# Performance work log

Measured on AMD Instinct MI355X. Metric: run time of the kernel, lower is better.

The kernel has to match this reference:

```python
import jax, jax.numpy as jnp
import numpy as np


def setup_inputs() -> dict:
    key = jax.random.key(0)
    k1, k2 = jax.random.split(key)
    N1, N2 = 16384, 16384
    pos1 = jax.random.normal(k1, (N1, 2), dtype=jnp.float32)
    pos2 = jax.random.normal(k2, (N2, 2), dtype=jnp.float32)
    return {"pos1": pos1, "pos2": pos2}


def reference(pos1, pos2):
    # pos1: [N1, 2], pos2: [N2, 2]
    diff = pos1[:, None, :] - pos2[None, :, :]          # [N1, N2, 2]
    dist = jnp.sqrt(jnp.sum(diff * diff, axis=2))       # [N1, N2]
    nearest = jnp.min(dist, axis=1)                     # [N1]
    return jnp.mean(nearest)
```

## Files before the change

### kernel.cpp

```cpp
#include <hip/hip_runtime.h>
#include <math.h>

#define N1 16384
#define N2 16384
#define BLOCK 256
#define PTS 8
#define I_BLOCKS (N1 / (BLOCK * PTS))
#define MAX_SLICE_N 1024

__global__ __launch_bounds__(BLOCK)
void nn_partial(const float2* __restrict__ pos1,
                const float2* __restrict__ pos2,
                float* __restrict__ partials,
                int slice_n) {
    __shared__ float4 sp[MAX_SLICE_N];
    const int ib = blockIdx.x;
    const int sl = blockIdx.y;
    const int t  = threadIdx.x;

    for (int j = t; j < slice_n; j += BLOCK) {
        float2 q = pos2[sl * slice_n + j];
        sp[j] = make_float4(-2.f * q.x, -2.f * q.y,
                            fmaf(q.x, q.x, q.y * q.y), 0.f);
    }
    __syncthreads();

    const int i0 = ib * (BLOCK * PTS) + t;
    float x[PTS], y[PTS], m[PTS];
#pragma unroll
    for (int k = 0; k < PTS; ++k) {
        float2 p = pos1[i0 + k * BLOCK];
        x[k] = p.x;
        y[k] = p.y;
        m[k] = 3.4e38f;
    }

#pragma unroll 2
    for (int j = 0; j < slice_n; ++j) {
        float4 q = sp[j];
#pragma unroll
        for (int k = 0; k < PTS; ++k) {
            float g = fmaf(x[k], q.x, fmaf(y[k], q.y, q.z));
            m[k] = fminf(m[k], g);
        }
    }

#pragma unroll
    for (int k = 0; k < PTS; ++k) {
        partials[(size_t)sl * N1 + i0 + k * BLOCK] = m[k];
    }
}

__global__ __launch_bounds__(BLOCK)
void nn_reduce(const float* __restrict__ partials,
               const float2* __restrict__ pos1,
               float* __restrict__ blocksums,
               int slices) {
    const int t = threadIdx.x;
    const int i = blockIdx.x * BLOCK + t;

    float m = 3.4e38f;
    for (int s = 0; s < slices; ++s) {
        m = fminf(m, partials[(size_t)s * N1 + i]);
    }
    float2 p = pos1[i];
    float d2 = fmaxf(fmaf(p.x, p.x, p.y * p.y) + m, 0.f);
    float sum = sqrtf(d2);

    for (int off = 32; off > 0; off >>= 1) {
        sum += __shfl_down(sum, off, 64);
    }
    __shared__ float wsum[BLOCK / 64];
    if ((t & 63) == 0) wsum[t >> 6] = sum;
    __syncthreads();
    if (t == 0) {
        float s = 0.f;
        for (int w = 0; w < BLOCK / 64; ++w) s += wsum[w];
        blocksums[blockIdx.x] = s;
    }
}

__global__ __launch_bounds__(64)
void nn_final(const float* __restrict__ blocksums,
              float* __restrict__ out, int nblk) {
    const int t = threadIdx.x;
    float sum = (t < nblk) ? blocksums[t] : 0.f;
    for (int off = 32; off > 0; off >>= 1) {
        sum += __shfl_down(sum, off, 64);
    }
    if (t == 0) out[0] = sum / (float)N1;
}

extern "C" void kernel_launch(void* const* d_in, const int* in_sizes, int n_in,
                              void* d_out, int out_size, void* d_ws, size_t ws_size,
                              hipStream_t stream) {
    const float2* pos1 = (const float2*)d_in[0];
    const float2* pos2 = (const float2*)d_in[1];
    float* out = (float*)d_out;
    float* partials = (float*)d_ws;

    const int nblk2 = N1 / BLOCK;
    int slices = 64;
    while (slices > 1 &&
           (size_t)slices * N1 * sizeof(float) + nblk2 * sizeof(float) > ws_size)
        slices >>= 1;
    while (N2 / slices > MAX_SLICE_N) slices <<= 1;
    const int slice_n = N2 / slices;

    float* blocksums = partials + (size_t)slices * N1;

    dim3 grid1(I_BLOCKS, slices);
    nn_partial<<<grid1, BLOCK, 0, stream>>>(pos1, pos2, partials, slice_n);
    nn_reduce<<<nblk2, BLOCK, 0, stream>>>(partials, pos1, blocksums, slices);
    nn_final<<<1, 64, 0, stream>>>(blocksums, out, nblk2);
}
```

Baseline: 87.41 us.

## Unroll inner loop by 8, double slice count, fold final reduce via ticket

The inner distance loop is unrolled by 8, with a batch of shared-memory points loaded up front to expose more ILP. The number of pos2 slices goes from 64 to 128, doubling grid parallelism for the partial kernel at the cost of more partial writes and reads in the reduce. The separate final kernel launch is removed: the last reduce block, detected with an atomic ticket that the first partial block resets, sums the block results. This saves one launch but adds an atomic and a threadfence.

Result: slower. 95.41 us (+9.2%).

```diff
diff --git a/kernel.cpp b/kernel.cpp
--- a/kernel.cpp
+++ b/kernel.cpp
@@ -7,16 +7,20 @@
 #define PTS 8
 #define I_BLOCKS (N1 / (BLOCK * PTS))
 #define MAX_SLICE_N 1024
+#define UJ 8
 
 __global__ __launch_bounds__(BLOCK)
 void nn_partial(const float2* __restrict__ pos1,
                 const float2* __restrict__ pos2,
                 float* __restrict__ partials,
+                unsigned int* __restrict__ ticket,
                 int slice_n) {
     __shared__ float4 sp[MAX_SLICE_N];
     const int ib = blockIdx.x;
     const int sl = blockIdx.y;
     const int t  = threadIdx.x;
+
+    if (ib == 0 && sl == 0 && t == 0) *ticket = 0;
 
     for (int j = t; j < slice_n; j += BLOCK) {
         float2 q = pos2[sl * slice_n + j];
@@ -35,13 +39,17 @@
         m[k] = 3.4e38f;
     }
 
-#pragma unroll 2
-    for (int j = 0; j < slice_n; ++j) {
-        float4 q = sp[j];
+    for (int j = 0; j < slice_n; j += UJ) {
+        float4 qb[UJ];
 #pragma unroll
-        for (int k = 0; k < PTS; ++k) {
-            float g = fmaf(x[k], q.x, fmaf(y[k], q.y, q.z));
-            m[k] = fminf(m[k], g);
+        for (int u = 0; u < UJ; ++u) qb[u] = sp[j + u];
+#pragma unroll
+        for (int u = 0; u < UJ; ++u) {
+#pragma unroll
+            for (int k = 0; k < PTS; ++k) {
+                float g = fmaf(x[k], qb[u].x, fmaf(y[k], qb[u].y, qb[u].z));
+                m[k] = fminf(m[k], g);
+            }
         }
     }
 
@@ -55,6 +63,8 @@
 void nn_reduce(const float* __restrict__ partials,
                const float2* __restrict__ pos1,
                float* __restrict__ blocksums,
+               unsigned int* __restrict__ ticket,
+               float* __restrict__ out,
                int slices) {
     const int t = threadIdx.x;
     const int i = blockIdx.x * BLOCK + t;
@@ -71,24 +81,26 @@
         sum += __shfl_down(sum, off, 64);
     }
     __shared__ float wsum[BLOCK / 64];
+    __shared__ int lastflag;
     if ((t & 63) == 0) wsum[t >> 6] = sum;
     __syncthreads();
     if (t == 0) {
         float s = 0.f;
         for (int w = 0; w < BLOCK / 64; ++w) s += wsum[w];
         blocksums[blockIdx.x] = s;
+        __threadfence();
+        unsigned int old = atomicAdd(ticket, 1u);
+        lastflag = (old == gridDim.x - 1) ? 1 : 0;
     }
-}
-
-__global__ __launch_bounds__(64)
-void nn_final(const float* __restrict__ blocksums,
-              float* __restrict__ out, int nblk) {
-    const int t = threadIdx.x;
-    float sum = (t < nblk) ? blocksums[t] : 0.f;
-    for (int off = 32; off > 0; off >>= 1) {
-        sum += __shfl_down(sum, off, 64);
+    __syncthreads();
+    if (lastflag && t < 64) {
+        volatile float* vb = (volatile float*)blocksums;
+        float v = vb[t];
+        for (int off = 32; off > 0; off >>= 1) {
+            v += __shfl_down(v, off, 64);
+        }
+        if (t == 0) out[0] = v / (float)N1;
     }
-    if (t == 0) out[0] = sum / (float)N1;
 }
 
 extern "C" void kernel_launch(void* const* d_in, const int* in_sizes, int n_in,
@@ -100,17 +112,17 @@
     float* partials = (float*)d_ws;
 
     const int nblk2 = N1 / BLOCK;
-    int slices = 64;
+    int slices = 128;
     while (slices > 1 &&
-           (size_t)slices * N1 * sizeof(float) + nblk2 * sizeof(float) > ws_size)
+           (size_t)slices * N1 * sizeof(float) + (nblk2 + 1) * sizeof(float) > ws_size)
         slices >>= 1;
     while (N2 / slices > MAX_SLICE_N) slices <<= 1;
     const int slice_n = N2 / slices;
 
     float* blocksums = partials + (size_t)slices * N1;
+    unsigned int* ticket = (unsigned int*)(blocksums + nblk2);
 
     dim3 grid1(I_BLOCKS, slices);
-    nn_partial<<<grid1, BLOCK, 0, stream>>>(pos1, pos2, partials, slice_n);
-    nn_reduce<<<nblk2, BLOCK, 0, stream>>>(partials, pos1, blocksums, slices);
-    nn_final<<<1, 64, 0, stream>>>(blocksums, out, nblk2);
+    nn_partial<<<grid1, BLOCK, 0, stream>>>(pos1, pos2, partials, ticket, slice_n);
+    nn_reduce<<<nblk2, BLOCK, 0, stream>>>(partials, pos1, blocksums, ticket, out, slices);
 }
```
